# Kernel tuning notes

Measured on AMD Instinct MI355X. Metric: run time of the kernel, lower is better.

## Reference

```python
import jax, jax.numpy as jnp
import numpy as np
from functools import partial

TAU = 2.0
V_TH = 1.0
T_STEPS = 10
SG_ALPHA = 4.0  # spikingjelly surrogate.Sigmoid default

@jax.custom_vjp
def spike(x):
    # Heaviside: 1 where x >= 0 (spikingjelly heaviside semantics)
    return (x >= 0).astype(x.dtype)

def _spike_fwd(x):
    return spike(x), x

def _spike_bwd(x, g):
    s = jax.nn.sigmoid(SG_ALPHA * x)
    return (g * SG_ALPHA * s * (1.0 - s),)

spike.defvjp(_spike_fwd, _spike_bwd)

def setup_inputs() -> dict:
    key = jax.random.key(0)
    ks = jax.random.split(key, 7)
    B, D_IN, H, A = 4096, 2048, 2048, 5
    def lin(k, fan_in, shape):
        bound = 1.0 / np.sqrt(fan_in)
        return jax.random.uniform(k, shape, jnp.float32, -bound, bound)
    return {
        "x": jax.random.normal(ks[0], (B, D_IN), jnp.float32),
        "W_in": lin(ks[1], D_IN, (D_IN, H)),
        "b_in": lin(ks[2], D_IN, (H,)),
        "W_snn": lin(ks[3], H, (H, H)),
        "b_snn": lin(ks[4], H, (H,)),
        "W_out": lin(ks[5], H, (H, A)),
        "b_out": lin(ks[6], H, (A,)),
    }

def lif_step(v, cur):
    # decay_input=True, v_reset=0: v <- v + (I - v)/tau; hard reset with detached spike
    v = v + (cur - v) / TAU
    s = spike(v - V_TH)
    v = (1.0 - jax.lax.stop_gradient(s)) * v
    return v, s

def reference(x, W_in, b_in, W_snn, b_snn, W_out, b_out):
    # input projection [B, H]
    h = x @ W_in + b_in
    # RSNNBlock: fc(h) is the same every timestep; LIF state carries across T steps
    cur = h @ W_snn + b_snn
    v0 = jnp.zeros_like(cur)
    _, spikes = jax.lax.scan(lambda v, _: lif_step(v, cur), v0, None, length=T_STEPS)
    rate = spikes.mean(axis=0)  # [B, H], mean firing rate
    # output head + single-step output LIF (fresh state v=0)
    pre = rate @ W_out + b_out  # [B, A]
    v_out, s_out = lif_step(jnp.zeros_like(pre), pre)
    return s_out
```

## Files before the change

### kernel.cpp

```cpp
#include <hip/hip_runtime.h>
#include <hip/hip_bf16.h>

static constexpr int BATCH = 4096;
static constexpr int DIN   = 2048;
static constexpr int HDIM  = 2048;
static constexpr int ADIM  = 5;

typedef __attribute__((ext_vector_type(8))) short short8;
typedef __attribute__((ext_vector_type(4))) float floatx4;

__device__ __forceinline__ unsigned short f2bf(float f) {
  unsigned int u = __float_as_uint(f);
  unsigned int r = (u + 0x7fffu + ((u >> 16) & 1u)) >> 16;
  return (unsigned short)r;
}
__device__ __forceinline__ float bf2f(unsigned short u) {
  return __uint_as_float(((unsigned int)u) << 16);
}

__global__ __launch_bounds__(256) void k_prep(const float* __restrict__ x,
                                              const float* __restrict__ W_in,
                                              const float* __restrict__ W_snn,
                                              unsigned short* __restrict__ xb,
                                              unsigned short* __restrict__ WinT,
                                              unsigned short* __restrict__ WsnT) {
  __shared__ float tl[32][33];
  const int b = blockIdx.x;
  if (b < 8192) {
    const int i = b * 256 + threadIdx.x;
    float4 v = ((const float4*)x)[i];
    ushort4 o;
    o.x = f2bf(v.x); o.y = f2bf(v.y); o.z = f2bf(v.z); o.w = f2bf(v.w);
    ((ushort4*)xb)[i] = o;
  } else {
    int bi = b - 8192;
    const float* src;
    unsigned short* dst;
    if (bi < 4096) { src = W_in; dst = WinT; }
    else           { src = W_snn; dst = WsnT; bi -= 4096; }
    const int bx = bi & 63, by = bi >> 6;
    const int c0 = bx * 32, r0 = by * 32;
    const int tx = threadIdx.x & 31, ty = threadIdx.x >> 5;
    #pragma unroll
    for (int s = 0; s < 32; s += 8)
      tl[ty + s][tx] = src[(size_t)(r0 + ty + s) * 2048 + (c0 + tx)];
    __syncthreads();
    #pragma unroll
    for (int s = 0; s < 32; s += 8)
      dst[(size_t)(c0 + ty + s) * 2048 + (r0 + tx)] = f2bf(tl[tx][ty + s]);
  }
}

template <int MODE>
__global__ __launch_bounds__(256, 2) void k_gemm(const unsigned short* __restrict__ Ag,
                                                 const unsigned short* __restrict__ BTg,
                                                 const float* __restrict__ bias,
                                                 unsigned short* __restrict__ outb,
                                                 int M, int N, int K) {
  constexpr int BK = 64;
  __shared__ unsigned short smem[2][16384];

  const int nbn = N / 128;
  const int nwg = gridDim.x;
  const int wg  = blockIdx.x;
  const int cpx = nwg >> 3;
  const int swz = (wg & 7) * cpx + (wg >> 3);
  const int bm = swz / nbn, bn = swz % nbn;
  const int m0 = bm * 128, n0 = bn * 128;

  const int t = threadIdx.x;
  const int l = t & 63;
  const int w = t >> 6;
  const int wc  = w & 1;
  const int kkh = w >> 1;

  const int srow = t >> 3;
  const int sg = (((t & 7) ^ (srow & 7)) << 3);
  const unsigned short* gA = Ag + (size_t)(m0 + srow) * K + sg;
  const unsigned short* gB = BTg + (size_t)(n0 + srow) * K + sg;

  const int NT = K / BK;

  auto stage = [&](int tt) {
    const int kt = tt * BK;
    char* base = (char*)&smem[tt & 1][0];
    #pragma unroll
    for (int j = 0; j < 4; ++j)
      __builtin_amdgcn_global_load_lds(
          (const __attribute__((address_space(1))) void*)(gA + (size_t)j * 32 * K + kt),
          (__attribute__((address_space(3))) void*)(base + t * 16 + j * 4096), 16, 0, 0);
    #pragma unroll
    for (int j = 0; j < 4; ++j)
      __builtin_amdgcn_global_load_lds(
          (const __attribute__((address_space(1))) void*)(gB + (size_t)j * 32 * K + kt),
          (__attribute__((address_space(3))) void*)(base + 16384 + t * 16 + j * 4096), 16, 0, 0);
  };

  const int soff = (((kkh << 2) | (l >> 4)) ^ (l & 7)) << 4;
  const int rA0 = (l & 15) * 128;
  const int rB0 = (wc * 64 + (l & 15)) * 128;

  floatx4 acc[8][4] = {};

  stage(0);
  __syncthreads();

  for (int tt = 0; tt < NT; ++tt) {
    if (tt + 1 < NT) stage(tt + 1);
    const char* Ab = (const char*)&smem[tt & 1][0];
    const char* Bb = Ab + 32768;
    short8 bf[4];
    #pragma unroll
    for (int j = 0; j < 4; ++j)
      bf[j] = *(const short8*)(Bb + rB0 + j * 2048 + soff);
    {
      short8 af[4];
      #pragma unroll
      for (int i = 0; i < 4; ++i)
        af[i] = *(const short8*)(Ab + rA0 + i * 2048 + soff);
      #pragma unroll
      for (int i = 0; i < 4; ++i)
        #pragma unroll
        for (int j = 0; j < 4; ++j)
          acc[i][j] = __builtin_amdgcn_mfma_f32_16x16x32_bf16(af[i], bf[j],
                                                              acc[i][j], 0, 0, 0);
    }
    {
      short8 af[4];
      #pragma unroll
      for (int i = 0; i < 4; ++i)
        af[i] = *(const short8*)(Ab + rA0 + (i + 4) * 2048 + soff);
      #pragma unroll
      for (int i = 0; i < 4; ++i)
        #pragma unroll
        for (int j = 0; j < 4; ++j)
          acc[i + 4][j] = __builtin_amdgcn_mfma_f32_16x16x32_bf16(af[i], bf[j],
                                                                  acc[i + 4][j], 0, 0, 0);
    }
    __syncthreads();
  }

  floatx4* xch = (floatx4*)&smem[0][0];
  if (kkh == 1) {
    #pragma unroll
    for (int i = 0; i < 8; ++i)
      #pragma unroll
      for (int j = 0; j < 4; ++j)
        xch[wc * 2048 + (i * 4 + j) * 64 + l] = acc[i][j];
  }
  __syncthreads();
  if (kkh == 0) {
    const int crow = m0 + ((l >> 4) << 2);
    const int ccol = n0 + wc * 64 + (l & 15);
    #pragma unroll
    for (int j = 0; j < 4; ++j) {
      const int col = ccol + j * 16;
      const float bv = bias[col];
      #pragma unroll
      for (int i = 0; i < 8; ++i) {
        floatx4 a = acc[i][j];
        floatx4 o = xch[wc * 2048 + (i * 4 + j) * 64 + l];
        const int row = crow + i * 16;
        #pragma unroll
        for (int r = 0; r < 4; ++r) {
          float v = a[r] + o[r] + bv;
          if (MODE == 1) {
            v = (v >= 2.0f)                ? 10.f
              : (v >= 1.3333333333333333f) ? 5.f
              : (v >= 1.1428571428571428f) ? 3.f
              : (v >= 1.0322580645161290f) ? 2.f
              : (v >= 1.0009775171065494f) ? 1.f : 0.f;
          }
          outb[(size_t)(row + r) * N + col] = f2bf(v);
        }
      }
    }
  }
}

__global__ __launch_bounds__(256) void k_head(const unsigned short* __restrict__ cntb,
                                              const float* __restrict__ Wout,
                                              const float* __restrict__ bout,
                                              float* __restrict__ out) {
  __shared__ float Wl[HDIM * ADIM];
  const int t = threadIdx.x;
  for (int i = t; i < HDIM * ADIM; i += 256) Wl[i] = Wout[i];
  __syncthreads();
  const int w = t >> 6, l = t & 63;
  const int row = blockIdx.x * 4 + w;
  const unsigned short* rp = cntb + (size_t)row * HDIM;
  float acc[ADIM] = {};
  #pragma unroll
  for (int it = 0; it < 4; ++it) {
    const int k0 = it * 512 + l * 8;
    short8 v = *(const short8*)(rp + k0);
    #pragma unroll
    for (int jj = 0; jj < 8; ++jj) {
      const float c = bf2f((unsigned short)v[jj]);
      const int k = k0 + jj;
      #pragma unroll
      for (int a = 0; a < ADIM; ++a) acc[a] += c * Wl[k * ADIM + a];
    }
  }
  #pragma unroll
  for (int a = 0; a < ADIM; ++a)
    #pragma unroll
    for (int off = 32; off >= 1; off >>= 1)
      acc[a] += __shfl_down(acc[a], off, 64);
  if (l == 0) {
    #pragma unroll
    for (int a = 0; a < ADIM; ++a) {
      const float pre = acc[a] * 0.1f + bout[a];
      const float vout = pre * 0.5f;
      out[(size_t)row * ADIM + a] = (vout - 1.0f >= 0.0f) ? 1.0f : 0.0f;
    }
  }
}

extern "C" void kernel_launch(void* const* d_in, const int* in_sizes, int n_in,
                              void* d_out, int out_size, void* d_ws, size_t ws_size,
                              hipStream_t stream) {
  const float* x     = (const float*)d_in[0];
  const float* W_in  = (const float*)d_in[1];
  const float* b_in  = (const float*)d_in[2];
  const float* W_snn = (const float*)d_in[3];
  const float* b_snn = (const float*)d_in[4];
  const float* W_out = (const float*)d_in[5];
  const float* b_out = (const float*)d_in[6];
  float* out = (float*)d_out;

  char* ws = (char*)d_ws;
  unsigned short* xb   = (unsigned short*)(ws);
  unsigned short* WinT = (unsigned short*)(ws + (size_t)16 * 1024 * 1024);
  unsigned short* WsnT = (unsigned short*)(ws + (size_t)24 * 1024 * 1024);
  unsigned short* hb   = (unsigned short*)(ws + (size_t)32 * 1024 * 1024);
  unsigned short* cntb = xb;

  k_prep<<<16384, 256, 0, stream>>>(x, W_in, W_snn, xb, WinT, WsnT);

  const int gblk = (BATCH / 128) * (HDIM / 128);
  k_gemm<0><<<gblk, 256, 0, stream>>>(xb, WinT, b_in, hb, BATCH, HDIM, DIN);

  k_gemm<1><<<gblk, 256, 0, stream>>>(hb, WsnT, b_snn, cntb, BATCH, HDIM, HDIM);

  k_head<<<BATCH / 4, 256, 0, stream>>>(cntb, W_out, b_out, out);
}
```

Baseline: 199.3 us.

## Fold input projection into recurrent weights via precomputed W_in·W_snn product

```diff
diff --git a/kernel.cpp b/kernel.cpp
--- a/kernel.cpp
+++ b/kernel.cpp
@@ -22,42 +22,153 @@
                                               const float* __restrict__ W_in,
                                               const float* __restrict__ W_snn,
                                               unsigned short* __restrict__ xb,
-                                              unsigned short* __restrict__ WinT,
-                                              unsigned short* __restrict__ WsnT) {
-  __shared__ float tl[32][33];
+                                              unsigned short* __restrict__ Winb,
+                                              unsigned short* __restrict__ WsnT,
+                                              float* __restrict__ bc) {
+  __shared__ float tl[64][65];
   const int b = blockIdx.x;
-  if (b < 8192) {
-    const int i = b * 256 + threadIdx.x;
-    float4 v = ((const float4*)x)[i];
+  if (b < 12288) {
+    const float4* src = (b < 8192) ? (const float4*)x : (const float4*)W_in;
+    ushort4* dst = (b < 8192) ? (ushort4*)xb : (ushort4*)Winb;
+    const int i = ((b < 8192) ? b : (b - 8192)) * 256 + threadIdx.x;
+    float4 v = src[i];
     ushort4 o;
     o.x = f2bf(v.x); o.y = f2bf(v.y); o.z = f2bf(v.z); o.w = f2bf(v.w);
-    ((ushort4*)xb)[i] = o;
+    dst[i] = o;
+  } else if (b < 13312) {
+    int bi = b - 12288;
+    const int bx = bi & 31, by = bi >> 5;
+    const int c0 = bx * 64, r0 = by * 64;
+    const int tx = threadIdx.x & 63, ty = threadIdx.x >> 6;
+    #pragma unroll
+    for (int s = 0; s < 64; s += 4)
+      tl[ty + s][tx] = W_snn[(size_t)(r0 + ty + s) * 2048 + (c0 + tx)];
+    __syncthreads();
+    #pragma unroll
+    for (int s = 0; s < 64; s += 4)
+      WsnT[(size_t)(c0 + ty + s) * 2048 + (r0 + tx)] = f2bf(tl[tx][ty + s]);
   } else {
-    int bi = b - 8192;
-    const float* src;
-    unsigned short* dst;
-    if (bi < 4096) { src = W_in; dst = WinT; }
-    else           { src = W_snn; dst = WsnT; bi -= 4096; }
-    const int bx = bi & 63, by = bi >> 6;
-    const int c0 = bx * 32, r0 = by * 32;
-    const int tx = threadIdx.x & 31, ty = threadIdx.x >> 5;
-    #pragma unroll
-    for (int s = 0; s < 32; s += 8)
-      tl[ty + s][tx] = src[(size_t)(r0 + ty + s) * 2048 + (c0 + tx)];
+    #pragma unroll
+    for (int s = 0; s < 8; ++s) bc[threadIdx.x + s * 256] = 0.0f;
+  }
+}
+
+__global__ __launch_bounds__(256) void k_bc(const float* __restrict__ b_in,
+                                            const float* __restrict__ W_snn,
+                                            float* __restrict__ bc) {
+  const int t = threadIdx.x;
+  const int k0 = blockIdx.x * 32;
+  float a[8] = {};
+  for (int k = k0; k < k0 + 32; ++k) {
+    const float bv = b_in[k];
+    const float* row = W_snn + (size_t)k * 2048;
+    #pragma unroll
+    for (int s = 0; s < 8; ++s) a[s] += bv * row[t + s * 256];
+  }
+  #pragma unroll
+  for (int s = 0; s < 8; ++s) atomicAdd(&bc[t + s * 256], a[s]);
+}
+
+__global__ __launch_bounds__(256, 2) void k_gemm_wc(const unsigned short* __restrict__ Ag,
+                                                    const unsigned short* __restrict__ BTg,
+                                                    unsigned short* __restrict__ outb) {
+  constexpr int K = 2048, N = 2048;
+  __shared__ unsigned short smem[2][12288];
+
+  const int nbn = N / 64;
+  const int nwg = gridDim.x;
+  const int wg  = blockIdx.x;
+  const int cpx = nwg >> 3;
+  const int swz = (wg & 7) * cpx + (wg >> 3);
+  const int bm = swz / nbn, bn = swz % nbn;
+  const int m0 = bm * 128, n0 = bn * 64;
+
+  const int t = threadIdx.x;
+  const int l = t & 63;
+  const int w = t >> 6;
+  const int wrow = w & 1;
+  const int kkh  = w >> 1;
+
+  const int srow = t >> 3;
+  const int sg = (((t & 7) ^ (srow & 7)) << 3);
+  const unsigned short* gA = Ag + (size_t)(m0 + srow) * K + sg;
+  const unsigned short* gB = BTg + (size_t)(n0 + srow) * K + sg;
+
+  auto stage = [&](int tt) {
+    const int kt = tt * 64;
+    char* base = (char*)&smem[tt & 1][0];
+    #pragma unroll
+    for (int j = 0; j < 4; ++j)
+      __builtin_amdgcn_global_load_lds(
+          (const __attribute__((address_space(1))) void*)(gA + (size_t)j * 32 * K + kt),
+          (__attribute__((address_space(3))) void*)(base + t * 16 + j * 4096), 16, 0, 0);
+    #pragma unroll
+    for (int j = 0; j < 2; ++j)
+      __builtin_amdgcn_global_load_lds(
+          (const __attribute__((address_space(1))) void*)(gB + (size_t)j * 32 * K + kt),
+          (__attribute__((address_space(3))) void*)(base + 16384 + t * 16 + j * 4096), 16, 0, 0);
+  };
+
+  const int soff = (((kkh << 2) | (l >> 4)) ^ (l & 7)) << 4;
+  const int rA0 = (wrow * 64 + (l & 15)) * 128 + soff;
+  const int rB0 = 16384 + (l & 15) * 128 + soff;
+
+  floatx4 acc[4][4] = {};
+
+  stage(0);
+  __syncthreads();
+
+  for (int tt = 0; tt < 32; ++tt) {
+    if (tt + 1 < 32) stage(tt + 1);
+    const char* Ab = (const char*)&smem[tt & 1][0];
+    short8 bf[4], af[4];
+    #pragma unroll
+    for (int j = 0; j < 4; ++j) bf[j] = *(const short8*)(Ab + rB0 + j * 2048);
+    #pragma unroll
+    for (int i = 0; i < 4; ++i) af[i] = *(const short8*)(Ab + rA0 + i * 2048);
+    #pragma unroll
+    for (int i = 0; i < 4; ++i)
+      #pragma unroll
+      for (int j = 0; j < 4; ++j)
+        acc[i][j] = __builtin_amdgcn_mfma_f32_16x16x32_bf16(af[i], bf[j],
+                                                            acc[i][j], 0, 0, 0);
     __syncthreads();
-    #pragma unroll
-    for (int s = 0; s < 32; s += 8)
-      dst[(size_t)(c0 + ty + s) * 2048 + (r0 + tx)] = f2bf(tl[tx][ty + s]);
-  }
-}
-
-template <int MODE>
-__global__ __launch_bounds__(256, 2) void k_gemm(const unsigned short* __restrict__ Ag,
-                                                 const unsigned short* __restrict__ BTg,
-                                                 const float* __restrict__ bias,
-                                                 unsigned short* __restrict__ outb,
-                                                 int M, int N, int K) {
-  constexpr int BK = 64;
+  }
+
+  floatx4* xch = (floatx4*)&smem[0][0];
+  if (kkh == 1) {
+    #pragma unroll
+    for (int i = 0; i < 4; ++i)
+      #pragma unroll
+      for (int j = 0; j < 4; ++j)
+        xch[wrow * 1024 + (i * 4 + j) * 64 + l] = acc[i][j];
+  }
+  __syncthreads();
+  if (kkh == 0) {
+    const int crow = m0 + wrow * 64 + ((l >> 4) << 2);
+    const int ccol = n0 + (l & 15);
+    #pragma unroll
+    for (int j = 0; j < 4; ++j) {
+      const int col = ccol + j * 16;
+      #pragma unroll
+      for (int i = 0; i < 4; ++i) {
+        floatx4 a = acc[i][j];
+        floatx4 o = xch[wrow * 1024 + (i * 4 + j) * 64 + l];
+        const int row = crow + i * 16;
+        #pragma unroll
+        for (int r = 0; r < 4; ++r)
+          outb[(size_t)(row + r) * N + col] = f2bf(a[r] + o[r]);
+      }
+    }
+  }
+}
+
+__global__ __launch_bounds__(256, 2) void k_gemm_lif(const unsigned short* __restrict__ Ag,
+                                                     const unsigned short* __restrict__ BTg,
+                                                     const float* __restrict__ bc,
+                                                     const float* __restrict__ b_snn,
+                                                     unsigned short* __restrict__ outb,
+                                                     int M, int N, int K) {
   __shared__ unsigned short smem[2][16384];
 
   const int nbn = N / 128;
@@ -79,10 +190,10 @@
   const unsigned short* gA = Ag + (size_t)(m0 + srow) * K + sg;
   const unsigned short* gB = BTg + (size_t)(n0 + srow) * K + sg;
 
-  const int NT = K / BK;
+  const int NT = K / 64;
 
   auto stage = [&](int tt) {
-    const int kt = tt * BK;
+    const int kt = tt * 64;
     char* base = (char*)&smem[tt & 1][0];
     #pragma unroll
     for (int j = 0; j < 4; ++j)
@@ -97,8 +208,8 @@
   };
 
   const int soff = (((kkh << 2) | (l >> 4)) ^ (l & 7)) << 4;
-  const int rA0 = (l & 15) * 128;
-  const int rB0 = (wc * 64 + (l & 15)) * 128;
+  const int rA0 = (l & 15) * 128 + soff;
+  const int rB0 = 32768 + (wc * 64 + (l & 15)) * 128 + soff;
 
   floatx4 acc[8][4] = {};
 
@@ -108,16 +219,13 @@
   for (int tt = 0; tt < NT; ++tt) {
     if (tt + 1 < NT) stage(tt + 1);
     const char* Ab = (const char*)&smem[tt & 1][0];
-    const char* Bb = Ab + 32768;
     short8 bf[4];
     #pragma unroll
-    for (int j = 0; j < 4; ++j)
-      bf[j] = *(const short8*)(Bb + rB0 + j * 2048 + soff);
+    for (int j = 0; j < 4; ++j) bf[j] = *(const short8*)(Ab + rB0 + j * 2048);
     {
       short8 af[4];
       #pragma unroll
-      for (int i = 0; i < 4; ++i)
-        af[i] = *(const short8*)(Ab + rA0 + i * 2048 + soff);
+      for (int i = 0; i < 4; ++i) af[i] = *(const short8*)(Ab + rA0 + i * 2048);
       #pragma unroll
       for (int i = 0; i < 4; ++i)
         #pragma unroll
@@ -128,8 +236,7 @@
     {
       short8 af[4];
       #pragma unroll
-      for (int i = 0; i < 4; ++i)
-        af[i] = *(const short8*)(Ab + rA0 + (i + 4) * 2048 + soff);
+      for (int i = 0; i < 4; ++i) af[i] = *(const short8*)(Ab + rA0 + (i + 4) * 2048);
       #pragma unroll
       for (int i = 0; i < 4; ++i)
         #pragma unroll
@@ -155,7 +262,7 @@
     #pragma unroll
     for (int j = 0; j < 4; ++j) {
       const int col = ccol + j * 16;
-      const float bv = bias[col];
+      const float bv = bc[col] + b_snn[col];
       #pragma unroll
       for (int i = 0; i < 8; ++i) {
         floatx4 a = acc[i][j];
@@ -164,13 +271,11 @@
         #pragma unroll
         for (int r = 0; r < 4; ++r) {
           float v = a[r] + o[r] + bv;
-          if (MODE == 1) {
-            v = (v >= 2.0f)                ? 10.f
-              : (v >= 1.3333333333333333f) ? 5.f
-              : (v >= 1.1428571428571428f) ? 3.f
-              : (v >= 1.0322580645161290f) ? 2.f
-              : (v >= 1.0009775171065494f) ? 1.f : 0.f;
-          }
+          v = (v >= 2.0f)                ? 10.f
+            : (v >= 1.3333333333333333f) ? 5.f
+            : (v >= 1.1428571428571428f) ? 3.f
+            : (v >= 1.0322580645161290f) ? 2.f
+            : (v >= 1.0009775171065494f) ? 1.f : 0.f;
           outb[(size_t)(row + r) * N + col] = f2bf(v);
         }
       }
@@ -187,32 +292,35 @@
   for (int i = t; i < HDIM * ADIM; i += 256) Wl[i] = Wout[i];
   __syncthreads();
   const int w = t >> 6, l = t & 63;
-  const int row = blockIdx.x * 4 + w;
-  const unsigned short* rp = cntb + (size_t)row * HDIM;
-  float acc[ADIM] = {};
   #pragma unroll
-  for (int it = 0; it < 4; ++it) {
-    const int k0 = it * 512 + l * 8;
-    short8 v = *(const short8*)(rp + k0);
-    #pragma unroll
-    for (int jj = 0; jj < 8; ++jj) {
-      const float c = bf2f((unsigned short)v[jj]);
-      const int k = k0 + jj;
-      #pragma unroll
-      for (int a = 0; a < ADIM; ++a) acc[a] += c * Wl[k * ADIM + a];
-    }
-  }
-  #pragma unroll
-  for (int a = 0; a < ADIM; ++a)
-    #pragma unroll
-    for (int off = 32; off >= 1; off >>= 1)
-      acc[a] += __shfl_down(acc[a], off, 64);
-  if (l == 0) {
-    #pragma unroll
-    for (int a = 0; a < ADIM; ++a) {
-      const float pre = acc[a] * 0.1f + bout[a];
-      const float vout = pre * 0.5f;
-      out[(size_t)row * ADIM + a] = (vout - 1.0f >= 0.0f) ? 1.0f : 0.0f;
+  for (int rr = 0; rr < 4; ++rr) {
+    const int row = blockIdx.x * 16 + w * 4 + rr;
+    const unsigned short* rp = cntb + (size_t)row * HDIM;
+    float acc[ADIM] = {};
+    #pragma unroll
+    for (int it = 0; it < 4; ++it) {
+      const int k0 = it * 512 + l * 8;
+      short8 v = *(const short8*)(rp + k0);
+      #pragma unroll
+      for (int jj = 0; jj < 8; ++jj) {
+        const float c = bf2f((unsigned short)v[jj]);
+        const int k = k0 + jj;
+        #pragma unroll
+        for (int a = 0; a < ADIM; ++a) acc[a] += c * Wl[k * ADIM + a];
+      }
+    }
+    #pragma unroll
+    for (int a = 0; a < ADIM; ++a)
+      #pragma unroll
+      for (int off = 32; off >= 1; off >>= 1)
+        acc[a] += __shfl_down(acc[a], off, 64);
+    if (l == 0) {
+      #pragma unroll
+      for (int a = 0; a < ADIM; ++a) {
+        const float pre = acc[a] * 0.1f + bout[a];
+        const float vout = pre * 0.5f;
+        out[(size_t)row * ADIM + a] = (vout - 1.0f >= 0.0f) ? 1.0f : 0.0f;
+      }
     }
   }
 }
@@ -231,17 +339,20 @@
 
   char* ws = (char*)d_ws;
   unsigned short* xb   = (unsigned short*)(ws);
-  unsigned short* WinT = (unsigned short*)(ws + (size_t)16 * 1024 * 1024);
+  unsigned short* Winb = (unsigned short*)(ws + (size_t)16 * 1024 * 1024);
   unsigned short* WsnT = (unsigned short*)(ws + (size_t)24 * 1024 * 1024);
-  unsigned short* hb   = (unsigned short*)(ws + (size_t)32 * 1024 * 1024);
-  unsigned short* cntb = xb;
-
-  k_prep<<<16384, 256, 0, stream>>>(x, W_in, W_snn, xb, WinT, WsnT);
-
-  const int gblk = (BATCH / 128) * (HDIM / 128);
-  k_gemm<0><<<gblk, 256, 0, stream>>>(xb, WinT, b_in, hb, BATCH, HDIM, DIN);
-
-  k_gemm<1><<<gblk, 256, 0, stream>>>(hb, WsnT, b_snn, cntb, BATCH, HDIM, HDIM);
-
-  k_head<<<BATCH / 4, 256, 0, stream>>>(cntb, W_out, b_out, out);
-}
+  unsigned short* WcT  = (unsigned short*)(ws + (size_t)32 * 1024 * 1024);
+  unsigned short* cntb = Winb;
+  float* bc = (float*)(ws + (size_t)47 * 1024 * 1024);
+
+  k_prep<<<13313, 256, 0, stream>>>(x, W_in, W_snn, xb, Winb, WsnT, bc);
+
+  k_bc<<<64, 256, 0, stream>>>(b_in, W_snn, bc);
+
+  k_gemm_wc<<<512, 256, 0, stream>>>(WsnT, Winb, WcT);
+
+  k_gemm_lif<<<512, 256, 0, stream>>>(xb, WcT, bc, b_snn, cntb,
+                                      BATCH, HDIM, DIN);
+
+  k_head<<<BATCH / 16, 256, 0, stream>>>(cntb, W_out, b_out, out);
+}
```

Measured after the change: 203.2 us. About the same (+1.9%).

## Fold W_in and W_snn into one combined weight to cut batch GEMMs

Applied to the files above, without the earlier changes.

```diff
diff --git a/kernel.cpp b/kernel.cpp
--- a/kernel.cpp
+++ b/kernel.cpp
@@ -22,85 +22,106 @@
                                               const float* __restrict__ W_in,
                                               const float* __restrict__ W_snn,
                                               unsigned short* __restrict__ xb,
-                                              unsigned short* __restrict__ WinT,
-                                              unsigned short* __restrict__ WsnT) {
-  __shared__ float tl[32][33];
+                                              unsigned short* __restrict__ Winb,
+                                              unsigned short* __restrict__ WsnT,
+                                              float* __restrict__ bc) {
+  __shared__ float tl[64][65];
   const int b = blockIdx.x;
-  if (b < 8192) {
-    const int i = b * 256 + threadIdx.x;
-    float4 v = ((const float4*)x)[i];
+  if (b < 12288) {
+    const float4* src = (b < 8192) ? (const float4*)x : (const float4*)W_in;
+    ushort4* dst = (b < 8192) ? (ushort4*)xb : (ushort4*)Winb;
+    const int i = ((b < 8192) ? b : (b - 8192)) * 256 + threadIdx.x;
+    float4 v = src[i];
     ushort4 o;
     o.x = f2bf(v.x); o.y = f2bf(v.y); o.z = f2bf(v.z); o.w = f2bf(v.w);
-    ((ushort4*)xb)[i] = o;
+    dst[i] = o;
+  } else if (b < 13312) {
+    int bi = b - 12288;
+    const int bx = bi & 31, by = bi >> 5;
+    const int c0 = bx * 64, r0 = by * 64;
+    const int tx = threadIdx.x & 63, ty = threadIdx.x >> 6;
+    #pragma unroll
+    for (int s = 0; s < 64; s += 4)
+      tl[ty + s][tx] = W_snn[(size_t)(r0 + ty + s) * 2048 + (c0 + tx)];
+    __syncthreads();
+    #pragma unroll
+    for (int s = 0; s < 64; s += 4)
+      WsnT[(size_t)(c0 + ty + s) * 2048 + (r0 + tx)] = f2bf(tl[tx][ty + s]);
   } else {
-    int bi = b - 8192;
-    const float* src;
-    unsigned short* dst;
-    if (bi < 4096) { src = W_in; dst = WinT; }
-    else           { src = W_snn; dst = WsnT; bi -= 4096; }
-    const int bx = bi & 63, by = bi >> 6;
-    const int c0 = bx * 32, r0 = by * 32;
-    const int tx = threadIdx.x & 31, ty = threadIdx.x >> 5;
-    #pragma unroll
-    for (int s = 0; s < 32; s += 8)
-      tl[ty + s][tx] = src[(size_t)(r0 + ty + s) * 2048 + (c0 + tx)];
-    __syncthreads();
-    #pragma unroll
-    for (int s = 0; s < 32; s += 8)
-      dst[(size_t)(c0 + ty + s) * 2048 + (r0 + tx)] = f2bf(tl[tx][ty + s]);
-  }
+    #pragma unroll
+    for (int s = 0; s < 8; ++s) bc[threadIdx.x + s * 256] = 0.0f;
+  }
+}
+
+__global__ __launch_bounds__(256) void k_bc(const float* __restrict__ b_in,
+                                            const float* __restrict__ W_snn,
+                                            float* __restrict__ bc) {
+  const int t = threadIdx.x;
+  const int k0 = blockIdx.x * 32;
+  float a[8] = {};
+  for (int k = k0; k < k0 + 32; ++k) {
+    const float bv = b_in[k];
+    const float* row = W_snn + (size_t)k * 2048;
+    #pragma unroll
+    for (int s = 0; s < 8; ++s) a[s] += bv * row[t + s * 256];
+  }
+  #pragma unroll
+  for (int s = 0; s < 8; ++s) atomicAdd(&bc[t + s * 256], a[s]);
 }
 
 template <int MODE>
-__global__ __launch_bounds__(256, 2) void k_gemm(const unsigned short* __restrict__ Ag,
+__global__ __launch_bounds__(512, 4) void k_gemm(const unsigned short* __restrict__ Ag,
                                                  const unsigned short* __restrict__ BTg,
-                                                 const float* __restrict__ bias,
-                                                 unsigned short* __restrict__ outb,
-                                                 int M, int N, int K) {
-  constexpr int BK = 64;
+                                                 const float* __restrict__ bias_a,
+                                                 const float* __restrict__ bias_b,
+                                                 unsigned short* __restrict__ outb) {
+  constexpr int Kfull = 2048;
+  constexpr int NT = (MODE == 0) ? 16 : 32;
   __shared__ unsigned short smem[2][16384];
 
-  const int nbn = N / 128;
   const int nwg = gridDim.x;
   const int wg  = blockIdx.x;
   const int cpx = nwg >> 3;
   const int swz = (wg & 7) * cpx + (wg >> 3);
-  const int bm = swz / nbn, bn = swz % nbn;
+  int kh, tile;
+  if (MODE == 0) { kh = swz >> 8; tile = swz & 255; }
+  else           { kh = 0;        tile = swz;       }
+  const int bm = tile >> 4, bn = tile & 15;
   const int m0 = bm * 128, n0 = bn * 128;
+  const int koff = kh << 10;
 
   const int t = threadIdx.x;
   const int l = t & 63;
   const int w = t >> 6;
-  const int wc  = w & 1;
-  const int kkh = w >> 1;
+  const int wn  = w & 1;
+  const int wm  = (w >> 1) & 1;
+  const int kkh = w >> 2;
 
   const int srow = t >> 3;
   const int sg = (((t & 7) ^ (srow & 7)) << 3);
-  const unsigned short* gA = Ag + (size_t)(m0 + srow) * K + sg;
-  const unsigned short* gB = BTg + (size_t)(n0 + srow) * K + sg;
-
-  const int NT = K / BK;
+  const unsigned short* gA = Ag + (size_t)(m0 + srow) * Kfull + koff + sg;
+  const unsigned short* gB = BTg + (size_t)(n0 + srow) * Kfull + koff + sg;
 
   auto stage = [&](int tt) {
-    const int kt = tt * BK;
+    const int kt = tt * 64;
     char* base = (char*)&smem[tt & 1][0];
     #pragma unroll
-    for (int j = 0; j < 4; ++j)
+    for (int j = 0; j < 2; ++j)
       __builtin_amdgcn_global_load_lds(
-          (const __attribute__((address_space(1))) void*)(gA + (size_t)j * 32 * K + kt),
-          (__attribute__((address_space(3))) void*)(base + t * 16 + j * 4096), 16, 0, 0);
-    #pragma unroll
-    for (int j = 0; j < 4; ++j)
+          (const __attribute__((address_space(1))) void*)(gA + (size_t)j * 64 * Kfull + kt),
+          (__attribute__((address_space(3))) void*)(base + t * 16 + j * 8192), 16, 0, 0);
+    #pragma unroll
+    for (int j = 0; j < 2; ++j)
       __builtin_amdgcn_global_load_lds(
-          (const __attribute__((address_space(1))) void*)(gB + (size_t)j * 32 * K + kt),
-          (__attribute__((address_space(3))) void*)(base + 16384 + t * 16 + j * 4096), 16, 0, 0);
+          (const __attribute__((address_space(1))) void*)(gB + (size_t)j * 64 * Kfull + kt),
+          (__attribute__((address_space(3))) void*)(base + 16384 + t * 16 + j * 8192), 16, 0, 0);
   };
 
   const int soff = (((kkh << 2) | (l >> 4)) ^ (l & 7)) << 4;
-  const int rA0 = (l & 15) * 128;
-  const int rB0 = (wc * 64 + (l & 15)) * 128;
-
-  floatx4 acc[8][4] = {};
+  const int rA0 = (wm * 64 + (l & 15)) * 128 + soff;
+  const int rB0 = 16384 + (wn * 64 + (l & 15)) * 128 + soff;
+
+  floatx4 acc[4][4] = {};
 
   stage(0);
   __syncthreads();
@@ -108,58 +129,42 @@
   for (int tt = 0; tt < NT; ++tt) {
     if (tt + 1 < NT) stage(tt + 1);
     const char* Ab = (const char*)&smem[tt & 1][0];
-    const char* Bb = Ab + 32768;
-    short8 bf[4];
-    #pragma unroll
-    for (int j = 0; j < 4; ++j)
-      bf[j] = *(const short8*)(Bb + rB0 + j * 2048 + soff);
-    {
-      short8 af[4];
-      #pragma unroll
-      for (int i = 0; i < 4; ++i)
-        af[i] = *(const short8*)(Ab + rA0 + i * 2048 + soff);
-      #pragma unroll
-      for (int i = 0; i < 4; ++i)
-        #pragma unroll
-        for (int j = 0; j < 4; ++j)
-          acc[i][j] = __builtin_amdgcn_mfma_f32_16x16x32_bf16(af[i], bf[j],
-                                                              acc[i][j], 0, 0, 0);
-    }
-    {
-      short8 af[4];
-      #pragma unroll
-      for (int i = 0; i < 4; ++i)
-        af[i] = *(const short8*)(Ab + rA0 + (i + 4) * 2048 + soff);
-      #pragma unroll
-      for (int i = 0; i < 4; ++i)
-        #pragma unroll
-        for (int j = 0; j < 4; ++j)
-          acc[i + 4][j] = __builtin_amdgcn_mfma_f32_16x16x32_bf16(af[i], bf[j],
-                                                                  acc[i + 4][j], 0, 0, 0);
-    }
+    short8 bf[4], af[4];
+    #pragma unroll
+    for (int j = 0; j < 4; ++j) bf[j] = *(const short8*)(Ab + rB0 + j * 2048);
+    #pragma unroll
+    for (int i = 0; i < 4; ++i) af[i] = *(const short8*)(Ab + rA0 + i * 2048);
+    #pragma unroll
+    for (int i = 0; i < 4; ++i)
+      #pragma unroll
+      for (int j = 0; j < 4; ++j)
+        acc[i][j] = __builtin_amdgcn_mfma_f32_16x16x32_bf16(af[i], bf[j],
+                                                            acc[i][j], 0, 0, 0);
     __syncthreads();
   }
 
   floatx4* xch = (floatx4*)&smem[0][0];
   if (kkh == 1) {
     #pragma unroll
-    for (int i = 0; i < 8; ++i)
+    for (int i = 0; i < 4; ++i)
       #pragma unroll
       for (int j = 0; j < 4; ++j)
-        xch[wc * 2048 + (i * 4 + j) * 64 + l] = acc[i][j];
+        xch[(w & 3) * 1024 + (i * 4 + j) * 64 + l] = acc[i][j];
   }
   __syncthreads();
   if (kkh == 0) {
-    const int crow = m0 + ((l >> 4) << 2);
-    const int ccol = n0 + wc * 64 + (l & 15);
+    unsigned short* outp = outb + (size_t)kh * 2048 * 2048;
+    const int crow = m0 + wm * 64 + ((l >> 4) << 2);
+    const int ccol = n0 + wn * 64 + (l & 15);
     #pragma unroll
     for (int j = 0; j < 4; ++j) {
       const int col = ccol + j * 16;
-      const float bv = bias[col];
-      #pragma unroll
-      for (int i = 0; i < 8; ++i) {
+      float bv = 0.0f;
+      if (MODE == 1) bv = bias_a[col] + bias_b[col];
+      #pragma unroll
+      for (int i = 0; i < 4; ++i) {
         floatx4 a = acc[i][j];
-        floatx4 o = xch[wc * 2048 + (i * 4 + j) * 64 + l];
+        floatx4 o = xch[w * 1024 + (i * 4 + j) * 64 + l];
         const int row = crow + i * 16;
         #pragma unroll
         for (int r = 0; r < 4; ++r) {
@@ -171,11 +176,24 @@
               : (v >= 1.0322580645161290f) ? 2.f
               : (v >= 1.0009775171065494f) ? 1.f : 0.f;
           }
-          outb[(size_t)(row + r) * N + col] = f2bf(v);
+          outp[(size_t)(row + r) * 2048 + col] = f2bf(v);
         }
       }
     }
   }
+}
+
+__global__ __launch_bounds__(256) void k_wcred(const ushort4* __restrict__ a,
+                                               const ushort4* __restrict__ b,
+                                               ushort4* __restrict__ o) {
+  const int i = blockIdx.x * 256 + threadIdx.x;
+  ushort4 x = a[i], y = b[i];
+  ushort4 r;
+  r.x = f2bf(bf2f(x.x) + bf2f(y.x));
+  r.y = f2bf(bf2f(x.y) + bf2f(y.y));
+  r.z = f2bf(bf2f(x.z) + bf2f(y.z));
+  r.w = f2bf(bf2f(x.w) + bf2f(y.w));
+  o[i] = r;
 }
 
 __global__ __launch_bounds__(256) void k_head(const unsigned short* __restrict__ cntb,
@@ -187,32 +205,35 @@
   for (int i = t; i < HDIM * ADIM; i += 256) Wl[i] = Wout[i];
   __syncthreads();
   const int w = t >> 6, l = t & 63;
-  const int row = blockIdx.x * 4 + w;
-  const unsigned short* rp = cntb + (size_t)row * HDIM;
-  float acc[ADIM] = {};
   #pragma unroll
-  for (int it = 0; it < 4; ++it) {
-    const int k0 = it * 512 + l * 8;
-    short8 v = *(const short8*)(rp + k0);
-    #pragma unroll
-    for (int jj = 0; jj < 8; ++jj) {
-      const float c = bf2f((unsigned short)v[jj]);
-      const int k = k0 + jj;
-      #pragma unroll
-      for (int a = 0; a < ADIM; ++a) acc[a] += c * Wl[k * ADIM + a];
+  for (int rr = 0; rr < 4; ++rr) {
+    const int row = blockIdx.x * 16 + w * 4 + rr;
+    const unsigned short* rp = cntb + (size_t)row * HDIM;
+    float acc[ADIM] = {};
+    #pragma unroll
+    for (int it = 0; it < 4; ++it) {
+      const int k0 = it * 512 + l * 8;
+      short8 v = *(const short8*)(rp + k0);
+      #pragma unroll
+      for (int jj = 0; jj < 8; ++jj) {
+        const float c = bf2f((unsigned short)v[jj]);
+        const int k = k0 + jj;
+        #pragma unroll
+        for (int a = 0; a < ADIM; ++a) acc[a] += c * Wl[k * ADIM + a];
+      }
     }
-  }
-  #pragma unroll
-  for (int a = 0; a < ADIM; ++a)
-    #pragma unroll
-    for (int off = 32; off >= 1; off >>= 1)
-      acc[a] += __shfl_down(acc[a], off, 64);
-  if (l == 0) {
-    #pragma unroll
-    for (int a = 0; a < ADIM; ++a) {
-      const float pre = acc[a] * 0.1f + bout[a];
-      const float vout = pre * 0.5f;
-      out[(size_t)row * ADIM + a] = (vout - 1.0f >= 0.0f) ? 1.0f : 0.0f;
+    #pragma unroll
+    for (int a = 0; a < ADIM; ++a)
+      #pragma unroll
+      for (int off = 32; off >= 1; off >>= 1)
+        acc[a] += __shfl_down(acc[a], off, 64);
+    if (l == 0) {
+      #pragma unroll
+      for (int a = 0; a < ADIM; ++a) {
+        const float pre = acc[a] * 0.1f + bout[a];
+        const float vout = pre * 0.5f;
+        out[(size_t)row * ADIM + a] = (vout - 1.0f >= 0.0f) ? 1.0f : 0.0f;
+      }
     }
   }
 }
@@ -231,17 +252,24 @@
 
   char* ws = (char*)d_ws;
   unsigned short* xb   = (unsigned short*)(ws);
-  unsigned short* WinT = (unsigned short*)(ws + (size_t)16 * 1024 * 1024);
+  unsigned short* Winb = (unsigned short*)(ws + (size_t)16 * 1024 * 1024);
   unsigned short* WsnT = (unsigned short*)(ws + (size_t)24 * 1024 * 1024);
-  unsigned short* hb   = (unsigned short*)(ws + (size_t)32 * 1024 * 1024);
-  unsigned short* cntb = xb;
-
-  k_prep<<<16384, 256, 0, stream>>>(x, W_in, W_snn, xb, WinT, WsnT);
-
-  const int gblk = (BATCH / 128) * (HDIM / 128);
-  k_gemm<0><<<gblk, 256, 0, stream>>>(xb, WinT, b_in, hb, BATCH, HDIM, DIN);
-
-  k_gemm<1><<<gblk, 256, 0, stream>>>(hb, WsnT, b_snn, cntb, BATCH, HDIM, HDIM);
-
-  k_head<<<BATCH / 4, 256, 0, stream>>>(cntb, W_out, b_out, out);
-}
+  unsigned short* Cp0  = (unsigned short*)(ws + (size_t)32 * 1024 * 1024);
+  unsigned short* Cp1  = (unsigned short*)(ws + (size_t)40 * 1024 * 1024);
+  unsigned short* WcT  = Cp0;
+  unsigned short* cntb = Winb;
+  float* bc = (float*)d_out;
+
+  k_prep<<<13313, 256, 0, stream>>>(x, W_in, W_snn, xb, Winb, WsnT, bc);
+
+  k_bc<<<64, 256, 0, stream>>>(b_in, W_snn, bc);
+
+  k_gemm<0><<<512, 512, 0, stream>>>(WsnT, Winb, nullptr, nullptr, Cp0);
+
+  k_wcred<<<4096, 256, 0, stream>>>((const ushort4*)Cp0, (const ushort4*)Cp1,
+                                    (ushort4*)WcT);
+
+  k_gemm<1><<<512, 512, 0, stream>>>(xb, WcT, bc, b_snn, cntb);
+
+  k_head<<<BATCH / 16, 256, 0, stream>>>(cntb, W_out, b_out, out);
+}
```

After: 196.7 us. About the same (-1.3%).
